# Kernel tuning notes

Measured on AMD Instinct MI355X. Metric: run time of the kernel, lower is better.

## Reference

```python
import jax, jax.numpy as jnp
import numpy as np

EMB = 256
HEADS = 4
HEAD_DIM = EMB // HEADS
N = 4096
M = 4096


def setup_inputs() -> dict:
    key = jax.random.key(0)
    ks = jax.random.split(key, 7)
    s = 1.0 / np.sqrt(EMB)  # keep logits in a sane range
    return {
        "A": jax.random.normal(ks[0], (N, EMB), jnp.float32),
        "B": jax.random.normal(ks[1], (M, EMB), jnp.float32),
        "Wq": jax.random.normal(ks[2], (EMB, EMB), jnp.float32) * s,
        "Wk": jax.random.normal(ks[3], (EMB, EMB), jnp.float32) * s,
        "Wv": jax.random.normal(ks[4], (EMB, EMB), jnp.float32) * s,
        "Wo": jax.random.normal(ks[5], (EMB, EMB), jnp.float32) * s,
        "bo": jnp.zeros((EMB,), jnp.float32),
    }


def _cross_attend(X, Y, Wq, Wk, Wv, Wo, bo):
    # X attends to Y. X:[n,emb], Y:[m,emb]
    scale = jnp.asarray(np.sqrt(HEAD_DIM), X.dtype)
    Q = (X @ Wq.T).reshape(X.shape[0], HEADS, HEAD_DIM)  # [n,h,d]
    K = (Y @ Wk.T).reshape(Y.shape[0], HEADS, HEAD_DIM)  # [m,h,d]
    V = (Y @ Wv.T).reshape(Y.shape[0], HEADS, HEAD_DIM)  # [m,h,d]
    scores = jnp.einsum("nhd,mhd->hnm", Q, K) / scale      # [h,n,m]
    attn = jax.nn.softmax(scores, axis=-1)                   # dropout p=0.0 -> identity
    ctx = jnp.einsum("hnm,mhd->nhd", attn, V).reshape(X.shape[0], EMB)
    return ctx @ Wo.T + bo + X                               # out proj + residual


def reference(A, B, Wq, Wk, Wv, Wo, bo):
    A_out = _cross_attend(A, B, Wq, Wk, Wv, Wo, bo)
    B_out = _cross_attend(B, A, Wq, Wk, Wv, Wo, bo)
    return (A_out, B_out)
```

## Files before the change

### kernel.cpp

```cpp
#include <hip/hip_runtime.h>
#include <hip/hip_bf16.h>
#include <math.h>

#define EMB 256
#define HEADS 4
#define HD 64
#define NTOK 4096

typedef __attribute__((ext_vector_type(8))) short bf16x8;
typedef __attribute__((ext_vector_type(4))) float f32x4;
typedef __attribute__((ext_vector_type(16))) float f32x16;
typedef __attribute__((ext_vector_type(2))) unsigned int uint2v;

#define MFMA16(a, b, c) __builtin_amdgcn_mfma_f32_16x16x32_bf16(a, b, c, 0, 0, 0)
#define MFMA32(a, b, c) __builtin_amdgcn_mfma_f32_32x32x16_bf16(a, b, c, 0, 0, 0)

static __device__ __forceinline__ ushort f2bf(float f) {
    __hip_bfloat16 h = __float2bfloat16(f);
    return *(ushort*)&h;
}
static __device__ __forceinline__ float ex2(float x) { return __builtin_amdgcn_exp2f(x); }
static __device__ __forceinline__ uint pkbf(float lo, float hi) {
    uint r;
    asm("v_cvt_pk_bf16_f32 %0, %1, %2" : "=v"(r) : "v"(lo), "v"(hi));
    return r;
}
static __device__ __forceinline__ float max3f(float a, float b, float c) {
    float r;
    asm("v_max3_f32 %0, %1, %2, %3" : "=v"(r) : "v"(a), "v"(b), "v"(c));
    return r;
}
static __device__ __forceinline__ float redmax32(float x) {
    uint xi = __float_as_uint(x);
    uint2v r = __builtin_amdgcn_permlane32_swap(xi, xi, false, false);
    return fmaxf(__uint_as_float(r[0]), __uint_as_float(r[1]));
}
static __device__ __forceinline__ float redsum32(float x) {
    uint xi = __float_as_uint(x);
    uint2v r = __builtin_amdgcn_permlane32_swap(xi, xi, false, false);
    return __uint_as_float(r[0]) + __uint_as_float(r[1]);
}
static __device__ __forceinline__ bf16x8 cvt8(float4 a, float4 b) {
    union { uint u[4]; bf16x8 h; } pk;
    pk.u[0] = pkbf(a.x, a.y);
    pk.u[1] = pkbf(a.z, a.w);
    pk.u[2] = pkbf(b.x, b.y);
    pk.u[3] = pkbf(b.z, b.w);
    return pk.h;
}
static __device__ __forceinline__ float bf2f(ushort u) {
    return __uint_as_float(((uint)u) << 16);
}

__global__ void cvtW(const float* __restrict__ Wq, const float* __restrict__ Wk,
                     const float* __restrict__ Wv, const float* __restrict__ Wo,
                     ushort* __restrict__ Wall) {
    const float* s = (blockIdx.y == 0) ? Wq : (blockIdx.y == 1) ? Wk : (blockIdx.y == 2) ? Wv : Wo;
    ushort* d = Wall + (size_t)blockIdx.y * 65536;
    int i = (blockIdx.x * 256 + threadIdx.x) * 4;
    float4 v = *(const float4*)(s + i);
    ushort4 o;
    o.x = f2bf(v.x); o.y = f2bf(v.y); o.z = f2bf(v.z); o.w = f2bf(v.w);
    *(ushort4*)(d + i) = o;
}

__global__ __launch_bounds__(256) void qkv_proj(const float* __restrict__ Xa,
                                                const float* __restrict__ Xb,
                                                const ushort* __restrict__ Wall,
                                                ushort* __restrict__ Q0, ushort* __restrict__ K1, ushort* __restrict__ Vt1,
                                                ushort* __restrict__ Q1, ushort* __restrict__ K0, ushort* __restrict__ Vt0) {
    int w = threadIdx.x >> 6, lane = threadIdx.x & 63;
    int lr = lane & 15, lg = lane >> 4;
    int z = blockIdx.z;
    int kind = (z < 3) ? z : z - 3;
    const float* X = (z < 3) ? Xa : Xb;
    ushort* Qo = (z < 3) ? Q0 : Q1;
    ushort* Ko = (z < 3) ? K1 : K0;
    ushort* Vto = (z < 3) ? Vt1 : Vt0;
    const ushort* W = Wall + (size_t)kind * 65536;
    int rbase = blockIdx.x * 64 + w * 16;
    int cbase = blockIdx.y * 64;

    f32x4 acc[4] = {};
#pragma unroll
    for (int kk = 0; kk < 256; kk += 32) {
        const float* xr = X + (size_t)(rbase + lr) * EMB + kk + lg * 8;
        bf16x8 a = cvt8(*(const float4*)xr, *(const float4*)(xr + 4));
#pragma unroll
        for (int cj = 0; cj < 4; ++cj) {
            bf16x8 b = *(const bf16x8*)(W + (size_t)(cbase + cj * 16 + lr) * EMB + kk + lg * 8);
            acc[cj] = MFMA16(a, b, acc[cj]);
        }
    }
    const float QS = 0.125f * 1.4426950408889634f;
#pragma unroll
    for (int cj = 0; cj < 4; ++cj)
#pragma unroll
        for (int j = 0; j < 4; ++j) {
            int R = rbase + lg * 4 + j;
            int col = cbase + cj * 16 + lr;
            float v = acc[cj][j];
            if (kind == 0) {
                Qo[(size_t)R * EMB + col] = f2bf(v * QS);
            } else if (kind == 1) {
                Ko[(size_t)R * EMB + col] = f2bf(v);
            } else {
                int h = col >> 6, d = col & 63;
                int Rp = (R & ~12) | ((R & 4) << 1) | ((R & 8) >> 1);
                Vto[(size_t)h * HD * NTOK + (size_t)d * NTOK + Rp] = f2bf(v);
            }
        }
}

__global__ __launch_bounds__(256, 4) void attn(const ushort* __restrict__ Q0,
                                               const ushort* __restrict__ K0,
                                               const ushort* __restrict__ Vt0,
                                               const ushort* __restrict__ Q1,
                                               const ushort* __restrict__ K1,
                                               const ushort* __restrict__ Vt1,
                                               ushort* __restrict__ Opart,
                                               float* __restrict__ ML) {
    __shared__ ushort lK[64 * 64];
    __shared__ ushort lV[64 * 64];

    int fb = blockIdx.x + 32 * blockIdx.y + 128 * blockIdx.z;
    int nf = (fb & 7) * 128 + (fb >> 3);
    int qt = nf & 31;
    int head = (nf >> 5) & 3;
    int z = nf >> 7;
    int dir = z >> 2, split = z & 3;
    int kv0 = split * 1024;

    const ushort* Q = dir ? Q1 : Q0;
    const ushort* K = dir ? K1 : K0;
    const ushort* Vt = dir ? Vt1 : Vt0;
    const ushort* Vth = Vt + (size_t)head * HD * NTOK;

    int wq = threadIdx.x >> 6;
    int lane = threadIdx.x & 63;
    int l31 = lane & 31, hi = lane >> 5;

    int qg = qt * 128 + wq * 32 + l31;
    bf16x8 qf[4];
#pragma unroll
    for (int ks = 0; ks < 4; ++ks)
        qf[ks] = *(const bf16x8*)(Q + (size_t)qg * EMB + head * 64 + ks * 16 + hi * 8);

    int srow = threadIdx.x >> 3, sseg = threadIdx.x & 7;
    int ssw = (sseg ^ ((srow >> 2) & 7)) * 8;

    uint4 rk0 = *(const uint4*)(K + (size_t)(kv0 + srow) * EMB + head * 64 + sseg * 8);
    uint4 rk1 = *(const uint4*)(K + (size_t)(kv0 + srow + 32) * EMB + head * 64 + sseg * 8);
    uint4 rv0 = *(const uint4*)(Vth + (size_t)srow * NTOK + kv0 + sseg * 8);
    uint4 rv1 = *(const uint4*)(Vth + (size_t)(srow + 32) * NTOK + kv0 + sseg * 8);

    float m = -1e30f, ls = 0.0f;
    f32x16 oacc0 = {};
    f32x16 oacc1 = {};
    int sw = (l31 >> 2) & 7;

    for (int t = 0; t < 16; ++t) {
        if (t) __syncthreads();
        *(uint4*)(&lK[srow * 64 + ssw]) = rk0;
        *(uint4*)(&lK[(srow + 32) * 64 + ssw]) = rk1;
        *(uint4*)(&lV[srow * 64 + ssw]) = rv0;
        *(uint4*)(&lV[(srow + 32) * 64 + ssw]) = rv1;
        __syncthreads();

        if (t < 15) {
            int nkv = kv0 + (t + 1) * 64;
            rk0 = *(const uint4*)(K + (size_t)(nkv + srow) * EMB + head * 64 + sseg * 8);
            rk1 = *(const uint4*)(K + (size_t)(nkv + srow + 32) * EMB + head * 64 + sseg * 8);
            rv0 = *(const uint4*)(Vth + (size_t)srow * NTOK + nkv + sseg * 8);
            rv1 = *(const uint4*)(Vth + (size_t)(srow + 32) * NTOK + nkv + sseg * 8);
        }

        f32x16 sA = {}, sB = {};
        __builtin_amdgcn_s_setprio(1);
#pragma unroll
        for (int ks = 0; ks < 4; ++ks) {
            bf16x8 ka = *(const bf16x8*)(&lK[l31 * 64 + ((ks * 2 + hi) ^ sw) * 8]);
            bf16x8 kb = *(const bf16x8*)(&lK[(32 + l31) * 64 + ((ks * 2 + hi) ^ sw) * 8]);
            sA = MFMA32(ka, qf[ks], sA);
            sB = MFMA32(kb, qf[ks], sB);
        }
        __builtin_amdgcn_s_setprio(0);

        float t0 = max3f(sA[0], sA[1], sA[2]);
        float t1 = max3f(sA[3], sA[4], sA[5]);
        float t2 = max3f(sA[6], sA[7], sA[8]);
        float t3 = max3f(sA[9], sA[10], sA[11]);
        float t4 = max3f(sA[12], sA[13], sA[14]);
        float t5 = max3f(sB[0], sB[1], sB[2]);
        float t6 = max3f(sB[3], sB[4], sB[5]);
        float t7 = max3f(sB[6], sB[7], sB[8]);
        float t8 = max3f(sB[9], sB[10], sB[11]);
        float t9 = max3f(sB[12], sB[13], sB[14]);
        float ta = fmaxf(sA[15], sB[15]);
        float u0 = max3f(t0, t1, t2);
        float u1 = max3f(t3, t4, t5);
        float u2 = max3f(t6, t7, t8);
        float u3 = fmaxf(t9, ta);
        float tmax = redmax32(fmaxf(max3f(u0, u1, u2), u3));

        if (__any(tmax > m + 8.0f)) {
            float mn = fmaxf(m, tmax);
            float sc = ex2(m - mn);
            m = mn;
            ls *= sc;
#pragma unroll
            for (int r = 0; r < 16; ++r) { oacc0[r] *= sc; oacc1[r] *= sc; }
        }

#pragma unroll
        for (int r = 0; r < 16; ++r) sA[r] = ex2(sA[r] - m);
#pragma unroll
        for (int r = 0; r < 16; ++r) sB[r] = ex2(sB[r] - m);

        float s1[16];
#pragma unroll
        for (int i = 0; i < 8; ++i) s1[i] = sA[2 * i] + sA[2 * i + 1];
#pragma unroll
        for (int i = 0; i < 8; ++i) s1[8 + i] = sB[2 * i] + sB[2 * i + 1];
#pragma unroll
        for (int w2 = 8; w2 >= 1; w2 >>= 1)
#pragma unroll
            for (int i = 0; i < 8; ++i)
                if (i < w2) s1[i] = s1[2 * i] + s1[2 * i + 1];
        ls += redsum32(s1[0]);

        bf16x8 pa[4];
#pragma unroll
        for (int ks = 0; ks < 4; ++ks) {
            union { uint u[4]; bf16x8 h; } pk;
#pragma unroll
            for (int j = 0; j < 4; ++j) {
                float lo = (ks < 2) ? sA[(ks & 1) * 8 + 2 * j] : sB[(ks & 1) * 8 + 2 * j];
                float hv = (ks < 2) ? sA[(ks & 1) * 8 + 2 * j + 1] : sB[(ks & 1) * 8 + 2 * j + 1];
                pk.u[j] = pkbf(lo, hv);
            }
            pa[ks] = pk.h;
        }

        __builtin_amdgcn_s_setprio(1);
#pragma unroll
        for (int ks = 0; ks < 4; ++ks) {
            bf16x8 va = *(const bf16x8*)(&lV[l31 * 64 + ((ks * 2 + hi) ^ sw) * 8]);
            bf16x8 vb = *(const bf16x8*)(&lV[(32 + l31) * 64 + ((ks * 2 + hi) ^ sw) * 8]);
            oacc0 = MFMA32(va, pa[ks], oacc0);
            oacc1 = MFMA32(vb, pa[ks], oacc1);
        }
        __builtin_amdgcn_s_setprio(0);
    }

    ushort* Ob = Opart + ((size_t)z * 4096 + qg) * 256 + head * 64;
#pragma unroll
    for (int r = 0; r < 16; ++r) {
        int crow = (r & 3) + 8 * (r >> 2) + 4 * hi;
        Ob[crow] = f2bf(oacc0[r]);
        Ob[32 + crow] = f2bf(oacc1[r]);
    }
    if (hi == 0) {
        float2* mlp = (float2*)ML;
        mlp[((size_t)z * 4 + head) * 4096 + qg] = make_float2(m, ls);
    }
}

__global__ __launch_bounds__(256) void out_proj(const ushort* __restrict__ Opart,
                                                const float* __restrict__ ML,
                                                const ushort* __restrict__ Wo,
                                                const float* __restrict__ bo,
                                                const float* __restrict__ A,
                                                const float* __restrict__ B,
                                                float* __restrict__ out) {
    int dir = blockIdx.z;
    const float* X = dir ? B : A;
    float* o = out + (size_t)dir * NTOK * EMB;

    int w = threadIdx.x >> 6, lane = threadIdx.x & 63;
    int lr = lane & 15, lg = lane >> 4;
    int rbase = blockIdx.x * 64 + w * 16;
    int cbase = blockIdx.y * 64;
    int R = rbase + lr;

    const float2* mlp = (const float2*)ML;
    float Wm[4][4];
#pragma unroll
    for (int h = 0; h < 4; ++h) {
        float2 ml[4];
        float M = -1e30f;
#pragma unroll
        for (int s = 0; s < 4; ++s) {
            ml[s] = mlp[((size_t)(dir * 4 + s) * 4 + h) * 4096 + R];
            M = fmaxf(M, ml[s].x);
        }
        float denom = 0.0f, a[4];
#pragma unroll
        for (int s = 0; s < 4; ++s) { a[s] = ex2(ml[s].x - M); denom += a[s] * ml[s].y; }
        float inv = 1.0f / denom;
#pragma unroll
        for (int s = 0; s < 4; ++s) Wm[h][s] = a[s] * inv;
    }

    const ushort* Or[4];
#pragma unroll
    for (int s = 0; s < 4; ++s)
        Or[s] = Opart + ((size_t)(dir * 4 + s) * 4096 + R) * 256;

    f32x4 acc[4] = {};
#pragma unroll
    for (int kk = 0; kk < 256; kk += 32) {
        int h = kk >> 6;
        bf16x8 xs0 = *(const bf16x8*)(Or[0] + kk + lg * 8);
        bf16x8 xs1 = *(const bf16x8*)(Or[1] + kk + lg * 8);
        bf16x8 xs2 = *(const bf16x8*)(Or[2] + kk + lg * 8);
        bf16x8 xs3 = *(const bf16x8*)(Or[3] + kk + lg * 8);
        float cv[8];
#pragma unroll
        for (int u = 0; u < 8; ++u) {
            cv[u] = Wm[h][0] * bf2f((ushort)xs0[u]) + Wm[h][1] * bf2f((ushort)xs1[u])
                  + Wm[h][2] * bf2f((ushort)xs2[u]) + Wm[h][3] * bf2f((ushort)xs3[u]);
        }
        float4 c0 = {cv[0], cv[1], cv[2], cv[3]};
        float4 c1 = {cv[4], cv[5], cv[6], cv[7]};
        bf16x8 a = cvt8(c0, c1);
#pragma unroll
        for (int cj = 0; cj < 4; ++cj) {
            bf16x8 b = *(const bf16x8*)(Wo + (size_t)(cbase + cj * 16 + lr) * EMB + kk + lg * 8);
            acc[cj] = MFMA16(a, b, acc[cj]);
        }
    }
#pragma unroll
    for (int cj = 0; cj < 4; ++cj)
#pragma unroll
        for (int j = 0; j < 4; ++j) {
            int Rr = rbase + lg * 4 + j;
            int col = cbase + cj * 16 + lr;
            o[(size_t)Rr * EMB + col] = acc[cj][j] + bo[col] + X[(size_t)Rr * EMB + col];
        }
}

extern "C" void kernel_launch(void* const* d_in, const int* in_sizes, int n_in,
                              void* d_out, int out_size, void* d_ws, size_t ws_size,
                              hipStream_t stream) {
    const float* A  = (const float*)d_in[0];
    const float* B  = (const float*)d_in[1];
    const float* Wq = (const float*)d_in[2];
    const float* Wk = (const float*)d_in[3];
    const float* Wv = (const float*)d_in[4];
    const float* Wo = (const float*)d_in[5];
    const float* bo = (const float*)d_in[6];
    float* out = (float*)d_out;

    ushort* ws = (ushort*)d_ws;
    const size_t TE = (size_t)NTOK * EMB;
    ushort* wall = ws;
    ushort* q0  = wall + 4 * 65536;
    ushort* q1  = q0 + TE;
    ushort* k0  = q1 + TE;
    ushort* k1  = k0 + TE;
    ushort* vt0 = k1 + TE;
    ushort* vt1 = vt0 + TE;
    ushort* Opart = vt1 + TE;
    float* ML = (float*)(Opart + (size_t)8 * 4096 * 256);

    cvtW<<<dim3(64, 4), 256, 0, stream>>>(Wq, Wk, Wv, Wo, wall);

    qkv_proj<<<dim3(64, 4, 6), 256, 0, stream>>>(A, B, wall, q0, k1, vt1, q1, k0, vt0);

    attn<<<dim3(32, 4, 8), 256, 0, stream>>>(q0, k0, vt0, q1, k1, vt1, Opart, ML);

    out_proj<<<dim3(64, 4, 2), 256, 0, stream>>>(Opart, ML, wall + 3 * 65536, bo, A, B, out);
}
```

Before: 113.4 us.

## Pre-convert inputs to bf16, double-buffer attention LDS tiles, vectorize output stores

Adds a kernel that converts A and B to bf16 once, so qkv_proj reads half the bytes and stops repeating the fp32-to-bf16 conversion in each of its 12 column/kind blocks. The attention kernel now ping-pongs between two K/V LDS buffers, which removes one __syncthreads per iteration. It also packs the output accumulator into uint2 stores instead of scalar ushort writes. The cost is an extra kernel launch, more workspace, and double the LDS per block, which may reduce occupancy.

```diff
diff --git a/kernel.cpp b/kernel.cpp
--- a/kernel.cpp
+++ b/kernel.cpp
@@ -50,6 +50,17 @@
 }
 static __device__ __forceinline__ float bf2f(ushort u) {
     return __uint_as_float(((uint)u) << 16);
+}
+
+__global__ void cvtAB(const float* __restrict__ A, const float* __restrict__ B,
+                      ushort* __restrict__ Ao, ushort* __restrict__ Bo) {
+    const float* s = blockIdx.y ? B : A;
+    ushort* d = blockIdx.y ? Bo : Ao;
+    int i = (blockIdx.x * 256 + threadIdx.x) * 4;
+    float4 v = *(const float4*)(s + i);
+    ushort4 o;
+    o.x = f2bf(v.x); o.y = f2bf(v.y); o.z = f2bf(v.z); o.w = f2bf(v.w);
+    *(ushort4*)(d + i) = o;
 }
 
 __global__ void cvtW(const float* __restrict__ Wq, const float* __restrict__ Wk,
@@ -64,8 +75,8 @@
     *(ushort4*)(d + i) = o;
 }
 
-__global__ __launch_bounds__(256) void qkv_proj(const float* __restrict__ Xa,
-                                                const float* __restrict__ Xb,
+__global__ __launch_bounds__(256) void qkv_proj(const ushort* __restrict__ Xa,
+                                                const ushort* __restrict__ Xb,
                                                 const ushort* __restrict__ Wall,
                                                 ushort* __restrict__ Q0, ushort* __restrict__ K1, ushort* __restrict__ Vt1,
                                                 ushort* __restrict__ Q1, ushort* __restrict__ K0, ushort* __restrict__ Vt0) {
@@ -73,7 +84,7 @@
     int lr = lane & 15, lg = lane >> 4;
     int z = blockIdx.z;
     int kind = (z < 3) ? z : z - 3;
-    const float* X = (z < 3) ? Xa : Xb;
+    const ushort* X = (z < 3) ? Xa : Xb;
     ushort* Qo = (z < 3) ? Q0 : Q1;
     ushort* Ko = (z < 3) ? K1 : K0;
     ushort* Vto = (z < 3) ? Vt1 : Vt0;
@@ -84,8 +95,7 @@
     f32x4 acc[4] = {};
 #pragma unroll
     for (int kk = 0; kk < 256; kk += 32) {
-        const float* xr = X + (size_t)(rbase + lr) * EMB + kk + lg * 8;
-        bf16x8 a = cvt8(*(const float4*)xr, *(const float4*)(xr + 4));
+        bf16x8 a = *(const bf16x8*)(X + (size_t)(rbase + lr) * EMB + kk + lg * 8);
 #pragma unroll
         for (int cj = 0; cj < 4; ++cj) {
             bf16x8 b = *(const bf16x8*)(W + (size_t)(cbase + cj * 16 + lr) * EMB + kk + lg * 8);
@@ -120,8 +130,8 @@
                                                const ushort* __restrict__ Vt1,
                                                ushort* __restrict__ Opart,
                                                float* __restrict__ ML) {
-    __shared__ ushort lK[64 * 64];
-    __shared__ ushort lV[64 * 64];
+    __shared__ ushort lK[2][64 * 64];
+    __shared__ ushort lV[2][64 * 64];
 
     int fb = blockIdx.x + 32 * blockIdx.y + 128 * blockIdx.z;
     int nf = (fb & 7) * 128 + (fb >> 3);
@@ -160,11 +170,13 @@
     int sw = (l31 >> 2) & 7;
 
     for (int t = 0; t < 16; ++t) {
-        if (t) __syncthreads();
-        *(uint4*)(&lK[srow * 64 + ssw]) = rk0;
-        *(uint4*)(&lK[(srow + 32) * 64 + ssw]) = rk1;
-        *(uint4*)(&lV[srow * 64 + ssw]) = rv0;
-        *(uint4*)(&lV[(srow + 32) * 64 + ssw]) = rv1;
+        int cur = t & 1;
+        ushort* lk = &lK[cur][0];
+        ushort* lv = &lV[cur][0];
+        *(uint4*)(&lk[srow * 64 + ssw]) = rk0;
+        *(uint4*)(&lk[(srow + 32) * 64 + ssw]) = rk1;
+        *(uint4*)(&lv[srow * 64 + ssw]) = rv0;
+        *(uint4*)(&lv[(srow + 32) * 64 + ssw]) = rv1;
         __syncthreads();
 
         if (t < 15) {
@@ -179,8 +191,8 @@
         __builtin_amdgcn_s_setprio(1);
 #pragma unroll
         for (int ks = 0; ks < 4; ++ks) {
-            bf16x8 ka = *(const bf16x8*)(&lK[l31 * 64 + ((ks * 2 + hi) ^ sw) * 8]);
-            bf16x8 kb = *(const bf16x8*)(&lK[(32 + l31) * 64 + ((ks * 2 + hi) ^ sw) * 8]);
+            bf16x8 ka = *(const bf16x8*)(&lk[l31 * 64 + ((ks * 2 + hi) ^ sw) * 8]);
+            bf16x8 kb = *(const bf16x8*)(&lk[(32 + l31) * 64 + ((ks * 2 + hi) ^ sw) * 8]);
             sA = MFMA32(ka, qf[ks], sA);
             sB = MFMA32(kb, qf[ks], sB);
         }
@@ -245,8 +257,8 @@
         __builtin_amdgcn_s_setprio(1);
 #pragma unroll
         for (int ks = 0; ks < 4; ++ks) {
-            bf16x8 va = *(const bf16x8*)(&lV[l31 * 64 + ((ks * 2 + hi) ^ sw) * 8]);
-            bf16x8 vb = *(const bf16x8*)(&lV[(32 + l31) * 64 + ((ks * 2 + hi) ^ sw) * 8]);
+            bf16x8 va = *(const bf16x8*)(&lv[l31 * 64 + ((ks * 2 + hi) ^ sw) * 8]);
+            bf16x8 vb = *(const bf16x8*)(&lv[(32 + l31) * 64 + ((ks * 2 + hi) ^ sw) * 8]);
             oacc0 = MFMA32(va, pa[ks], oacc0);
             oacc1 = MFMA32(vb, pa[ks], oacc1);
         }
@@ -255,10 +267,14 @@
 
     ushort* Ob = Opart + ((size_t)z * 4096 + qg) * 256 + head * 64;
 #pragma unroll
-    for (int r = 0; r < 16; ++r) {
-        int crow = (r & 3) + 8 * (r >> 2) + 4 * hi;
-        Ob[crow] = f2bf(oacc0[r]);
-        Ob[32 + crow] = f2bf(oacc1[r]);
+    for (int g = 0; g < 4; ++g) {
+        uint2 o0, o1;
+        o0.x = pkbf(oacc0[4 * g + 0], oacc0[4 * g + 1]);
+        o0.y = pkbf(oacc0[4 * g + 2], oacc0[4 * g + 3]);
+        o1.x = pkbf(oacc1[4 * g + 0], oacc1[4 * g + 1]);
+        o1.y = pkbf(oacc1[4 * g + 2], oacc1[4 * g + 3]);
+        *(uint2*)(&Ob[8 * g + 4 * hi]) = o0;
+        *(uint2*)(&Ob[32 + 8 * g + 4 * hi]) = o1;
     }
     if (hi == 0) {
         float2* mlp = (float2*)ML;
@@ -355,7 +371,9 @@
     ushort* ws = (ushort*)d_ws;
     const size_t TE = (size_t)NTOK * EMB;
     ushort* wall = ws;
-    ushort* q0  = wall + 4 * 65536;
+    ushort* abf = wall + 4 * 65536;
+    ushort* bbf = abf + TE;
+    ushort* q0  = bbf + TE;
     ushort* q1  = q0 + TE;
     ushort* k0  = q1 + TE;
     ushort* k1  = k0 + TE;
@@ -364,9 +382,10 @@
     ushort* Opart = vt1 + TE;
     float* ML = (float*)(Opart + (size_t)8 * 4096 * 256);
 
+    cvtAB<<<dim3(1024, 2), 256, 0, stream>>>(A, B, abf, bbf);
     cvtW<<<dim3(64, 4), 256, 0, stream>>>(Wq, Wk, Wv, Wo, wall);
 
-    qkv_proj<<<dim3(64, 4, 6), 256, 0, stream>>>(A, B, wall, q0, k1, vt1, q1, k0, vt0);
+    qkv_proj<<<dim3(64, 4, 6), 256, 0, stream>>>(abf, bbf, wall, q0, k1, vt1, q1, k0, vt0);
 
     attn<<<dim3(32, 4, 8), 256, 0, stream>>>(q0, k0, vt0, q1, k1, vt1, Opart, ML);
 
```

Measured after the change: 108.4 us. -4.4%, faster.
